# Kernel tuning notes

Measured on AMD Instinct MI355X. Metric: run time of the kernel, lower is better.

## Reference

```python
import jax, jax.numpy as jnp
import numpy as np

H = 512          # hidden_size
HALF = 256       # hidden_size // 2 (RGCN feature dim)
NHEAD = 8
NLAYER = 12
NBLOCK = 2
NENT = 50000
NREL = 12
NBASES = 8
NEDGE = 500000
TXTD = 768       # raw text/image feature dim
BATCH, ELEN, SLEN = 32, 50, 128


def setup_inputs() -> dict:
    key = jax.random.key(0)
    ks = jax.random.split(key, 40)
    def p(i, shape, scale=0.02):
        return jax.random.normal(ks[i], shape, jnp.float32) * scale
    inp = {
        'entity_ids': jax.random.randint(ks[0], (BATCH, ELEN), 0, NENT),
        'token_embeds': jax.random.normal(ks[1], (BATCH, SLEN, H), jnp.float32),
        'edge_index': jax.random.randint(ks[2], (2, NEDGE), 0, NENT),
        'edge_type': jax.random.randint(ks[3], (NEDGE,), 0, NREL),
        'node_embeds': p(4, (NENT, HALF)),
        'rgcn_basis': p(5, (NBASES, HALF, HALF)),
        'rgcn_comp': p(6, (NREL, NBASES), 0.3),
        'rgcn_root': p(7, (HALF, HALF)),
        'rgcn_bias': p(8, (HALF,)),
        'kg_proj_w': p(9, (HALF, H)), 'kg_proj_b': p(10, (H,)),
        'text_proj_w': p(11, (TXTD, H)), 'text_proj_b': p(12, (H,)),
        'image_proj_w': p(13, (TXTD, H)), 'image_proj_b': p(14, (H,)),
        'cq_w': p(15, (H, H)), 'cq_b': p(16, (H,)),
        'kgk_w': p(17, (H, H)), 'kgk_b': p(18, (H,)),
        'imk_w': p(19, (H, H)), 'imk_b': p(20, (H,)),
        'txk_w': p(21, (H, H)), 'txk_b': p(22, (H,)),
        'pp1_w1': p(23, (H, HALF)), 'pp1_b1': p(24, (HALF,)),
        'pp1_w2': p(25, (HALF, H)), 'pp1_b2': p(26, (H,)),
        'pp2_w': p(27, (H, NLAYER * NBLOCK * H)), 'pp2_b': p(28, (NLAYER * NBLOCK * H,)),
        'text_embeds_init': p(29, (NENT, TXTD), 1.0),
        'image_embeds_init': p(30, (NENT, TXTD), 1.0),
    }
    return inp


def _rgcn(x, edge_index, edge_type, basis, comp, root, bias):
    # PyG RGCNConv with basis decomposition, aggr='mean', root weight + bias.
    # mean_{e: rel=r, dst=i}(x[src_e] @ W_r) == (mean_{e}(x[src_e])) @ W_r, so we
    # aggregate raw features per (dst, relation) segment then apply W_r once per node.
    N = x.shape[0]
    src, dst = edge_index[0], edge_index[1]
    seg = dst * NREL + edge_type                      # combined (node, relation) key
    msgs = x[src]                                     # [E, HALF] gather
    agg = jax.ops.segment_sum(msgs, seg, num_segments=N * NREL)
    cnt = jax.ops.segment_sum(jnp.ones((src.shape[0],), x.dtype), seg, num_segments=N * NREL)
    mean = (agg / jnp.maximum(cnt, 1.0)[:, None]).reshape(N, NREL, HALF)
    w_rel = jnp.einsum('rb,bio->rio', comp, basis)    # [R, HALF, HALF]
    out = jnp.einsum('nri,rio->no', mean, w_rel) + x @ root + bias
    return out


def reference(entity_ids, token_embeds, edge_index, edge_type, node_embeds,
              rgcn_basis, rgcn_comp, rgcn_root, rgcn_bias,
              kg_proj_w, kg_proj_b, text_proj_w, text_proj_b,
              image_proj_w, image_proj_b, cq_w, cq_b,
              kgk_w, kgk_b, imk_w, imk_b, txk_w, txk_b,
              pp1_w1, pp1_b1, pp1_w2, pp1_b2, pp2_w, pp2_b,
              text_embeds_init, image_embeds_init):
    kg_all = _rgcn(node_embeds, edge_index, edge_type, rgcn_basis, rgcn_comp, rgcn_root, rgcn_bias)
    kg_all = kg_all @ kg_proj_w + kg_proj_b           # [N, H]
    kg_feat = kg_all[entity_ids]                      # [B, L, H]
    text_feat = text_embeds_init[entity_ids] @ text_proj_w + text_proj_b
    image_feat = image_embeds_init[entity_ids] @ image_proj_w + image_proj_b
    # context-guided fusion
    q = (jnp.mean(token_embeds, axis=1) @ cq_w + cq_b)[:, None, :]   # [B, 1, H]
    kg_s = jnp.sum(q * (kg_feat @ kgk_w + kgk_b), -1, keepdims=True)
    img_s = jnp.sum(q * (image_feat @ imk_w + imk_b), -1, keepdims=True)
    txt_s = jnp.sum(q * (text_feat @ txk_w + txk_b), -1, keepdims=True)
    w = jax.nn.softmax(jnp.concatenate([kg_s, img_s, txt_s], axis=-1), axis=-1)
    fused = w[..., 0:1] * kg_feat + w[..., 1:2] * image_feat + w[..., 2:3] * text_feat
    # prompt expansion
    h = jax.nn.relu(fused @ pp1_w1 + pp1_b1) @ pp1_w2 + pp1_b2 + fused
    p = h @ pp2_w + pp2_b                             # [B, L, NLAYER*NBLOCK*H]
    B, L = entity_ids.shape
    p = p.reshape(B, L, NLAYER, NBLOCK, NHEAD, H // NHEAD)
    p = jnp.transpose(p, (2, 3, 0, 4, 1, 5))          # [layer, block, B, head, L, head_dim]
    loss_cl = jnp.float32(0.0)                        # output_entity=False path
    return p, loss_cl
```

## Files before the change

### kernel.cpp

```cpp
#include <hip/hip_runtime.h>

#define HDIM 512
#define HALF 256
#define NRELS 12
#define NBASES 8
#define NLAYERS 12
#define NBLOCKS 2
#define NHEADS 8
#define NENTS 50000
#define TXTD 768
#define BATCH 32
#define ELEN 50
#define SLEN 128
#define NPOS (BATCH * ELEN)
#define NSEG (NPOS * NRELS)
#define BCAP 64

typedef unsigned short u16;
typedef __attribute__((ext_vector_type(8))) __bf16 bf16x8;
typedef __attribute__((ext_vector_type(4))) float f32x4;

__device__ __forceinline__ u16 f2bf(float f) {
    unsigned int u = __float_as_uint(f);
    unsigned int r = (u + 0x7FFFu + ((u >> 16) & 1u)) >> 16;
    return (u16)r;
}
__device__ __forceinline__ float bf2f(u16 v) {
    return __uint_as_float(((unsigned int)v) << 16);
}

#define ASYNC_COPY16(g, l)                                                              \
    __builtin_amdgcn_global_load_lds((const __attribute__((address_space(1))) void*)(g), \
                                     (__attribute__((address_space(3))) unsigned int*)(l), 16, 0, 0)

__global__ void init_kernel(int* __restrict__ map, int* __restrict__ segcnt,
                            int* __restrict__ nuniq, float* __restrict__ zb,
                            const float* __restrict__ kgb, const float* __restrict__ imb,
                            const float* __restrict__ txb, u16* __restrict__ SW,
                            const float* __restrict__ rgcn_bias,
                            const float* __restrict__ kg_proj_w,
                            const float* __restrict__ kg_proj_b,
                            float* __restrict__ biasC, float* __restrict__ out_last) {
    int blk = blockIdx.x;
    int t = threadIdx.x;
    if (blk >= 128) {
        int n = (blk - 128) * 256 + t;
        float acc = kg_proj_b[n];
        for (int c = 0; c < HALF; ++c) acc += rgcn_bias[c] * kg_proj_w[(size_t)c * HDIM + n];
        biasC[n] = acc;
        return;
    }
    int tid = blk * 256 + t;
    const int nt = 128 * 256;
    int4 m4 = {-1, -1, -1, -1};
    for (int i = tid; i < NENTS / 4; i += nt) ((int4*)map)[i] = m4;
    int4 z4 = {0, 0, 0, 0};
    for (int i = tid; i < NSEG / 4; i += nt) ((int4*)segcnt)[i] = z4;
    for (int i = tid; i < 2304; i += nt) zb[i] = 0.f;
    if (tid < HDIM) {
        SW[(size_t)1536 * HDIM + tid] = f2bf(kgb[tid]);
        SW[(size_t)1537 * HDIM + tid] = f2bf(imb[tid]);
        SW[(size_t)1538 * HDIM + tid] = f2bf(txb[tid]);
    }
    if (tid == 0) { *nuniq = 0; *out_last = 0.f; }
}

__global__ void dedup_kernel(const int* __restrict__ eid, int* __restrict__ map,
                             int* __restrict__ uniq, int* __restrict__ nuniq) {
    int i = blockIdx.x * blockDim.x + threadIdx.x;
    if (i >= NPOS) return;
    int n = eid[i];
    int old = atomicCAS(&map[n], -1, -2);
    if (old == -1) {
        int idx = atomicAdd(nuniq, 1);
        uniq[idx] = n;
        __threadfence();
        map[n] = idx;
    }
}

struct PrepArgs {
    const float* src[12];
    u16* dst[12];
};

__global__ __launch_bounds__(256) void midprep_kernel(
    const float* __restrict__ tok, u16* __restrict__ TMEAN,
    const int* __restrict__ uniq, const int* __restrict__ nuniq,
    const float* __restrict__ txi, const float* __restrict__ imi,
    u16* __restrict__ TXIN, u16* __restrict__ IMIN,
    const int* __restrict__ ei, const int* __restrict__ et, const int* __restrict__ map,
    int* __restrict__ segcnt, int* __restrict__ bucket, int E, PrepArgs a) {
    int blk = blockIdx.x;
    int t = threadIdx.x;
    if (blk < 64) {
        int b = blk >> 1;
        int col = (blk & 1) * 256 + t;
        float s = 0.f;
        for (int si = 0; si < SLEN; ++si) s += tok[((size_t)b * SLEN + si) * HDIM + col];
        TMEAN[(size_t)b * HDIM + col] = f2bf(s * (1.0f / SLEN));
    } else if (blk < 352) {
        if (t >= TXTD / 4) return;
        int nu = *nuniq;
        for (int u = blk - 64; u < NPOS; u += 288) {
            if (u >= nu) {
                ushort4 z = {0, 0, 0, 0};
                ((ushort4*)(TXIN + (size_t)u * TXTD))[t] = z;
                ((ushort4*)(IMIN + (size_t)u * TXTD))[t] = z;
                continue;
            }
            int n = uniq[u];
            float4 v = ((const float4*)(txi + (size_t)n * TXTD))[t];
            ushort4 o;
            o.x = f2bf(v.x); o.y = f2bf(v.y); o.z = f2bf(v.z); o.w = f2bf(v.w);
            ((ushort4*)(TXIN + (size_t)u * TXTD))[t] = o;
            v = ((const float4*)(imi + (size_t)n * TXTD))[t];
            o.x = f2bf(v.x); o.y = f2bf(v.y); o.z = f2bf(v.z); o.w = f2bf(v.w);
            ((ushort4*)(IMIN + (size_t)u * TXTD))[t] = o;
        }
    } else if (blk < 1024) {
        const int* __restrict__ dstA = ei + E;
        int tid0 = (blk - 352) * 256 + t;
        const int stride = 672 * 256;
        for (int e = tid0; e < E; e += stride) {
            int c = map[dstA[e]];
            if (c >= 0) {
                int seg = c * NRELS + et[e];
                int p = atomicAdd(&segcnt[seg], 1);
                if (p < BCAP) bucket[seg * BCAP + p] = ei[e];
            }
        }
    } else {
        constexpr int NN[7]  = {512, 512, 512, 256, 512, 12288, 512};
        constexpr int LDT[7] = {256, 768, 768, 512, 256, 512, 512};
        constexpr int BASE[13] = {0, 128, 512, 896, 1024, 1152, 7296,
                                  7552, 8064, 8128, 8384, 8640, 8896};
        __shared__ u16 tb[32][33];
        int bid = blk - 1024;
        int op = 0;
        #pragma unroll
        for (int i = 1; i < 12; ++i)
            if (bid >= BASE[i]) op = i;
        int idx = bid - BASE[op];
        if (op < 7) {
            int Nv = 0, ldt = 0;
            #pragma unroll
            for (int i = 0; i < 7; ++i)
                if (op == i) { Nv = NN[i]; ldt = LDT[i]; }
            int ncols = Nv / 32;
            int n0 = (idx % ncols) * 32, k0 = (idx / ncols) * 32;
            const float* W = a.src[op];
            u16* WT = a.dst[op];
            int tx = t & 31, ty = t >> 5;
            #pragma unroll
            for (int i = ty; i < 32; i += 8)
                tb[i][tx] = f2bf(W[(size_t)(k0 + i) * Nv + n0 + tx]);
            __syncthreads();
            #pragma unroll
            for (int i = ty; i < 32; i += 8)
                WT[(size_t)(n0 + i) * ldt + k0 + tx] = tb[tx][i];
        } else {
            int e = idx * 1024 + t * 4;
            float4 v = *(const float4*)(a.src[op] + e);
            ushort4 o;
            o.x = f2bf(v.x); o.y = f2bf(v.y); o.z = f2bf(v.z); o.w = f2bf(v.w);
            *(ushort4*)(a.dst[op] + e) = o;
        }
    }
}

template <int BM, int BN, int WM, int WN, bool SCATTER>
__device__ __forceinline__ void gemm_body(const u16* __restrict__ A, const u16* __restrict__ BT,
                                          const float* __restrict__ bias,
                                          void* __restrict__ Cout, int M, int N, int K,
                                          int bx, int by, bool outbf) {
    constexpr int MF = WM / 16, NF = WN / 16;
    constexpr int NWC = BN / WN;
    __shared__ u16 ldsA[BM][64];
    __shared__ u16 ldsB[BN][64];
    const int tid = threadIdx.x;
    const int lane = tid & 63;
    const int wv = tid >> 6;
    const int m0 = by * BM;
    const int n0 = bx * BN;
    const int wr = wv / NWC, wc = wv % NWC;
    const int srow = lane >> 3;
    const int sslot = lane & 7;

    f32x4 acc[MF][NF];
    #pragma unroll
    for (int i = 0; i < MF; ++i)
        #pragma unroll
        for (int j = 0; j < NF; ++j)
            #pragma unroll
            for (int r = 0; r < 4; ++r) acc[i][j][r] = 0.f;

    for (int k0 = 0; k0 < K; k0 += 64) {
        #pragma unroll
        for (int i = 0; i < BM / 32; ++i) {
            int R = wv * (BM / 4) + i * 8 + srow;
            int gm = m0 + R;
            gm = gm < M ? gm : M - 1;
            int s = sslot ^ (R & 7);
            ASYNC_COPY16(A + (size_t)gm * K + k0 + s * 8, &ldsA[wv * (BM / 4) + i * 8][0]);
        }
        #pragma unroll
        for (int i = 0; i < BN / 32; ++i) {
            int R = wv * (BN / 4) + i * 8 + srow;
            int s = sslot ^ (R & 7);
            ASYNC_COPY16(BT + (size_t)(n0 + R) * K + k0 + s * 8, &ldsB[wv * (BN / 4) + i * 8][0]);
        }
        __syncthreads();
        #pragma unroll
        for (int ks = 0; ks < 2; ++ks) {
            bf16x8 af[MF], bf[NF];
            int kg = ks * 4 + (lane >> 4);
            int rl = lane & 15;
            #pragma unroll
            for (int i = 0; i < MF; ++i) {
                int row = wr * WM + i * 16 + rl;
                af[i] = *(const bf16x8*)&ldsA[row][(kg ^ (row & 7)) * 8];
            }
            #pragma unroll
            for (int j = 0; j < NF; ++j) {
                int row = wc * WN + j * 16 + rl;
                bf[j] = *(const bf16x8*)&ldsB[row][(kg ^ (row & 7)) * 8];
            }
            #pragma unroll
            for (int i = 0; i < MF; ++i)
                #pragma unroll
                for (int j = 0; j < NF; ++j)
                    acc[i][j] = __builtin_amdgcn_mfma_f32_16x16x32_bf16(af[i], bf[j], acc[i][j], 0, 0, 0);
        }
        __syncthreads();
    }

    const int rl = lane & 15, rg = lane >> 4;
    #pragma unroll
    for (int i = 0; i < MF; ++i) {
        #pragma unroll
        for (int j = 0; j < NF; ++j) {
            int col = n0 + wc * WN + j * 16 + rl;
            float bv = bias[col];
            #pragma unroll
            for (int r = 0; r < 4; ++r) {
                int row = m0 + wr * WM + i * 16 + rg * 4 + r;
                if (row >= M) continue;
                float x = acc[i][j][r] + bv;
                if (SCATTER) {
                    int layer = col >> 10, blk = (col >> 9) & 1, head = (col >> 6) & 7, hd = col & 63;
                    int bb = row / ELEN, ll = row - bb * ELEN;
                    size_t oi = (((((size_t)layer * NBLOCKS + blk) * BATCH + bb) * NHEADS + head) * ELEN + ll) * 64 + hd;
                    ((float*)Cout)[oi] = x;
                } else if (outbf) {
                    ((u16*)Cout)[(size_t)row * N + col] = f2bf(x);
                } else {
                    ((float*)Cout)[(size_t)row * N + col] = x;
                }
            }
        }
    }
}

__global__ __launch_bounds__(256) void build_kernel(
    const int* __restrict__ segcnt, const int* __restrict__ bucket,
    const int* __restrict__ uniq, const int* __restrict__ nuniq,
    const float* __restrict__ comp, const float* __restrict__ x, u16* __restrict__ MBX,
    const u16* __restrict__ TMEAN, const u16* __restrict__ CQT,
    const float* __restrict__ cq_b, u16* __restrict__ QB,
    const u16* __restrict__ KGT, const u16* __restrict__ W1f,
    const float* __restrict__ ZB, u16* __restrict__ WC) {
    int blk = blockIdx.x;
    if (blk >= NPOS) {
        const u16 *A, *BT;
        const float* bias;
        u16* C;
        int M, N, K, bx, by;
        if (blk >= NPOS + 8) {
            int i = blk - (NPOS + 8);
            A = KGT; BT = W1f; bias = ZB; C = WC;
            M = HDIM; N = 2304; K = HALF; bx = i % 36; by = i / 36;
        } else {
            A = TMEAN; BT = CQT; bias = cq_b; C = QB;
            M = BATCH; N = HDIM; K = HDIM; bx = blk - NPOS; by = 0;
        }
        gemm_body<64, 64, 32, 32, false>(A, BT, bias, C, M, N, K, bx, by, true);
        return;
    }
    int u = blk;
    int i = threadIdx.x;
    __shared__ float sc[NRELS * NBASES];
    if (i < NRELS * NBASES) sc[i] = comp[i];
    __syncthreads();
    u16* row = MBX + (size_t)u * 2304;
    int nu = *nuniq;
    if (u >= nu) {
        for (int b = 0; b < NBASES + 1; ++b) row[b * HALF + i] = 0;
        return;
    }
    float mr[NRELS];
    #pragma unroll
    for (int r = 0; r < NRELS; ++r) {
        int seg = u * NRELS + r;
        int c = segcnt[seg];
        int n = min(c, BCAP);
        float acc = 0.f;
        for (int e = 0; e < n; ++e) {
            int s = bucket[seg * BCAP + e];
            acc += x[(size_t)s * HALF + i];
        }
        mr[r] = acc * (1.f / fmaxf((float)c, 1.f));
    }
    #pragma unroll
    for (int b = 0; b < NBASES; ++b) {
        float a = 0.f;
        #pragma unroll
        for (int r = 0; r < NRELS; ++r) a += sc[r * NBASES + b] * mr[r];
        row[b * HALF + i] = f2bf(a);
    }
    row[NBASES * HALF + i] = f2bf(x[(size_t)uniq[u] * HALF + i]);
}

struct Proj4Args {
    const u16 *MBX, *WC, *TXIN, *TXT, *IMIN, *IMT, *QB, *SW;
    const float *biasC, *txb, *imb, *ZB;
    u16 *KGU, *TXU, *IMU;
    float* QP;
};
__global__ __launch_bounds__(256) void proj4_kernel(Proj4Args a) {
    int b = blockIdx.x;
    const u16 *A, *BT;
    const float* bias;
    void* C;
    int M, N, K, bx, by;
    bool obf;
    if (b < 200) {
        A = a.MBX; BT = a.WC; bias = a.biasC; C = a.KGU;
        M = NPOS; N = HDIM; K = 2304; bx = b % 8; by = b / 8; obf = true;
    } else if (b < 400) {
        int i = b - 200;
        A = a.TXIN; BT = a.TXT; bias = a.txb; C = a.TXU;
        M = NPOS; N = HDIM; K = TXTD; bx = i % 8; by = i / 8; obf = true;
    } else if (b < 600) {
        int i = b - 400;
        A = a.IMIN; BT = a.IMT; bias = a.imb; C = a.IMU;
        M = NPOS; N = HDIM; K = TXTD; bx = i % 8; by = i / 8; obf = true;
    } else {
        A = a.QB; BT = a.SW; bias = a.ZB; C = a.QP;
        M = BATCH; N = 1600; K = HDIM; bx = b - 600; by = 0; obf = false;
    }
    gemm_body<64, 64, 32, 32, false>(A, BT, bias, C, M, N, K, bx, by, obf);
}

__global__ __launch_bounds__(256) void tail_kernel(
    const int* __restrict__ eid, const int* __restrict__ map,
    const u16* __restrict__ KGU, const u16* __restrict__ IMU, const u16* __restrict__ TXU,
    const float* __restrict__ qp,
    const u16* __restrict__ W1T, const float* __restrict__ pp1_b1,
    const u16* __restrict__ W2T, const float* __restrict__ pp1_b2,
    u16* __restrict__ Hh) {
    __shared__ u16 FUS[16][520];
    __shared__ u16 P1s[16][264];
    const int bm0 = blockIdx.x * 16;
    const int lane = threadIdx.x & 63;
    const int wv = threadIdx.x >> 6;

    for (int rr = wv; rr < 16; rr += 4) {
        int bl = bm0 + rr;
        int b = bl / ELEN;
        int u = map[eid[bl]];
        const u16* kg = KGU + (size_t)u * HDIM;
        const u16* im = IMU + (size_t)u * HDIM;
        const u16* tx = TXU + (size_t)u * HDIM;
        const float* qrow = qp + (size_t)b * 1600;
        float pkg = 0.f, pim = 0.f, ptx = 0.f;
        for (int e = lane; e < HDIM; e += 64) {
            pkg += bf2f(kg[e]) * qrow[e];
            pim += bf2f(im[e]) * qrow[512 + e];
            ptx += bf2f(tx[e]) * qrow[1024 + e];
        }
        #pragma unroll
        for (int off = 32; off; off >>= 1) {
            pkg += __shfl_down(pkg, off);
            pim += __shfl_down(pim, off);
            ptx += __shfl_down(ptx, off);
        }
        float w0, w1, w2;
        if (lane == 0) {
            float av = pkg + qrow[1536];
            float c1 = pim + qrow[1537];
            float c2 = ptx + qrow[1538];
            float mx = fmaxf(av, fmaxf(c1, c2));
            float ea = __expf(av - mx), eb = __expf(c1 - mx), ec = __expf(c2 - mx);
            float inv = 1.f / (ea + eb + ec);
            w0 = ea * inv; w1 = eb * inv; w2 = ec * inv;
        }
        w0 = __shfl(w0, 0); w1 = __shfl(w1, 0); w2 = __shfl(w2, 0);
        for (int e = lane; e < HDIM; e += 64) {
            float v = w0 * bf2f(kg[e]) + w1 * bf2f(im[e]) + w2 * bf2f(tx[e]);
            FUS[rr][e] = f2bf(v);
        }
    }
    __syncthreads();

    {
        const int rl = lane & 15;
        const int kgrp = lane >> 4;
        f32x4 acc[4];
        #pragma unroll
        for (int j = 0; j < 4; ++j)
            #pragma unroll
            for (int r = 0; r < 4; ++r) acc[j][r] = 0.f;
        for (int kk = 0; kk < 512; kk += 32) {
            int k8 = kk + kgrp * 8;
            bf16x8 af = *(const bf16x8*)&FUS[rl][k8];
            bf16x8 bf[4];
            #pragma unroll
            for (int j = 0; j < 4; ++j) {
                int n = wv * 64 + j * 16 + rl;
                bf[j] = *(const bf16x8*)&W1T[(size_t)n * 512 + k8];
            }
            #pragma unroll
            for (int j = 0; j < 4; ++j)
                acc[j] = __builtin_amdgcn_mfma_f32_16x16x32_bf16(af, bf[j], acc[j], 0, 0, 0);
        }
        const int rg = lane >> 4;
        #pragma unroll
        for (int j = 0; j < 4; ++j) {
            int col = wv * 64 + j * 16 + rl;
            float bv = pp1_b1[col];
            #pragma unroll
            for (int r = 0; r < 4; ++r) {
                int row = rg * 4 + r;
                P1s[row][col] = f2bf(fmaxf(acc[j][r] + bv, 0.f));
            }
        }
    }
    __syncthreads();

    {
        const int rl = lane & 15;
        const int kgrp = lane >> 4;
        f32x4 acc[8];
        #pragma unroll
        for (int j = 0; j < 8; ++j)
            #pragma unroll
            for (int r = 0; r < 4; ++r) acc[j][r] = 0.f;
        for (int kk = 0; kk < 256; kk += 32) {
            int k8 = kk + kgrp * 8;
            bf16x8 af = *(const bf16x8*)&P1s[rl][k8];
            bf16x8 bf[8];
            #pragma unroll
            for (int j = 0; j < 8; ++j) {
                int n = wv * 128 + j * 16 + rl;
                bf[j] = *(const bf16x8*)&W2T[(size_t)n * 256 + k8];
            }
            #pragma unroll
            for (int j = 0; j < 8; ++j)
                acc[j] = __builtin_amdgcn_mfma_f32_16x16x32_bf16(af, bf[j], acc[j], 0, 0, 0);
        }
        const int rg = lane >> 4;
        #pragma unroll
        for (int j = 0; j < 8; ++j) {
            int col = wv * 128 + j * 16 + rl;
            float bv = pp1_b2[col];
            #pragma unroll
            for (int r = 0; r < 4; ++r) {
                int row = rg * 4 + r;
                float v = acc[j][r] + bv + bf2f(FUS[row][col]);
                Hh[(size_t)(bm0 + row) * HDIM + col] = f2bf(v);
            }
        }
    }
}

__global__ __launch_bounds__(256)
void pp2_kernel(const u16* __restrict__ A, const u16* __restrict__ BT,
                const float* __restrict__ bias, void* __restrict__ Cout,
                int M, int N, int K) {
    gemm_body<128, 128, 64, 64, true>(A, BT, bias, Cout, M, N, K, blockIdx.x, blockIdx.y, false);
}

extern "C" void kernel_launch(void* const* d_in, const int* in_sizes, int n_in,
                              void* d_out, int out_size, void* d_ws, size_t ws_size,
                              hipStream_t stream) {
    const int* entity_ids = (const int*)d_in[0];
    const float* token_embeds = (const float*)d_in[1];
    const int* edge_index = (const int*)d_in[2];
    const int* edge_type = (const int*)d_in[3];
    const float* node_embeds = (const float*)d_in[4];
    const float* rgcn_basis = (const float*)d_in[5];
    const float* rgcn_comp = (const float*)d_in[6];
    const float* rgcn_root = (const float*)d_in[7];
    const float* rgcn_bias = (const float*)d_in[8];
    const float* kg_proj_w = (const float*)d_in[9];
    const float* kg_proj_b = (const float*)d_in[10];
    const float* text_proj_w = (const float*)d_in[11];
    const float* text_proj_b = (const float*)d_in[12];
    const float* image_proj_w = (const float*)d_in[13];
    const float* image_proj_b = (const float*)d_in[14];
    const float* cq_w = (const float*)d_in[15];
    const float* cq_b = (const float*)d_in[16];
    const float* kgk_w = (const float*)d_in[17];
    const float* imk_w = (const float*)d_in[19];
    const float* txk_w = (const float*)d_in[21];
    const float* pp1_w1 = (const float*)d_in[23];
    const float* pp1_b1 = (const float*)d_in[24];
    const float* pp1_w2 = (const float*)d_in[25];
    const float* pp1_b2 = (const float*)d_in[26];
    const float* pp2_w = (const float*)d_in[27];
    const float* pp2_b = (const float*)d_in[28];
    const float* text_init = (const float*)d_in[29];
    const float* image_init = (const float*)d_in[30];

    const int E = in_sizes[3];

    size_t off = 0;
    auto alloc = [&](size_t bytes) { size_t o = off; off += (bytes + 255) & ~(size_t)255; return o; };
    char* ws = (char*)d_ws;
    size_t map_o  = alloc((size_t)NENTS * 4);
    size_t nun_o  = alloc(4);
    size_t unq_o  = alloc((size_t)NPOS * 4);
    size_t scnt_o = alloc((size_t)NSEG * 4);
    size_t bkt_o  = alloc((size_t)NSEG * BCAP * 4);
    size_t mbx_o  = alloc((size_t)NPOS * 2304 * 2);
    size_t w1f_o  = alloc((size_t)2304 * HALF * 2);
    size_t wc_o   = alloc((size_t)HDIM * 2304 * 2);
    size_t bc_o   = alloc((size_t)HDIM * 4);
    size_t kgt_o  = alloc((size_t)HDIM * HALF * 2);
    size_t kgu_o  = alloc((size_t)NPOS * HDIM * 2);
    size_t txin_o = alloc((size_t)NPOS * TXTD * 2);
    size_t imin_o = alloc((size_t)NPOS * TXTD * 2);
    size_t txt_o  = alloc((size_t)HDIM * TXTD * 2);
    size_t imt_o  = alloc((size_t)HDIM * TXTD * 2);
    size_t txu_o  = alloc((size_t)NPOS * HDIM * 2);
    size_t imu_o  = alloc((size_t)NPOS * HDIM * 2);
    size_t tm_o   = alloc((size_t)BATCH * HDIM * 2);
    size_t qb_o   = alloc((size_t)BATCH * HDIM * 2);
    size_t cqt_o  = alloc((size_t)HDIM * HDIM * 2);
    size_t sw_o   = alloc((size_t)1600 * HDIM * 2);
    size_t qp_o   = alloc((size_t)BATCH * 1600 * 4);
    size_t zb_o   = alloc((size_t)2304 * 4);
    size_t w1t_o  = alloc((size_t)HALF * HDIM * 2);
    size_t w2t_o  = alloc((size_t)HDIM * HALF * 2);
    size_t h_o    = alloc((size_t)NPOS * HDIM * 2);
    size_t pp2t_o = alloc((size_t)12288 * HDIM * 2);
    if (off > ws_size) return;

    int* map = (int*)(ws + map_o);
    int* nuniq = (int*)(ws + nun_o);
    int* uniq = (int*)(ws + unq_o);
    int* segcnt = (int*)(ws + scnt_o);
    int* bucket = (int*)(ws + bkt_o);
    u16* MBX = (u16*)(ws + mbx_o);
    u16* W1f = (u16*)(ws + w1f_o);
    u16* WC  = (u16*)(ws + wc_o);
    float* biasC = (float*)(ws + bc_o);
    u16* KGT = (u16*)(ws + kgt_o);
    u16* KGU = (u16*)(ws + kgu_o);
    u16* TXIN = (u16*)(ws + txin_o);
    u16* IMIN = (u16*)(ws + imin_o);
    u16* TXT = (u16*)(ws + txt_o);
    u16* IMT = (u16*)(ws + imt_o);
    u16* TXU = (u16*)(ws + txu_o);
    u16* IMU = (u16*)(ws + imu_o);
    u16* TMEAN = (u16*)(ws + tm_o);
    u16* QB  = (u16*)(ws + qb_o);
    u16* CQT = (u16*)(ws + cqt_o);
    u16* SW  = (u16*)(ws + sw_o);
    float* QP  = (float*)(ws + qp_o);
    float* ZB  = (float*)(ws + zb_o);
    u16* W1T = (u16*)(ws + w1t_o);
    u16* W2T = (u16*)(ws + w2t_o);
    u16* Hh  = (u16*)(ws + h_o);
    u16* PP2T = (u16*)(ws + pp2t_o);
    float* OUT = (float*)d_out;

    init_kernel<<<130, 256, 0, stream>>>(map, segcnt, nuniq, ZB,
                                         (const float*)d_in[18], (const float*)d_in[20],
                                         (const float*)d_in[22], SW,
                                         rgcn_bias, kg_proj_w, kg_proj_b, biasC,
                                         OUT + (out_size - 1));
    dedup_kernel<<<(NPOS + 255) / 256, 256, 0, stream>>>(entity_ids, map, uniq, nuniq);
    PrepArgs pa;
    pa.src[0] = kg_proj_w;    pa.dst[0] = KGT;
    pa.src[1] = text_proj_w;  pa.dst[1] = TXT;
    pa.src[2] = image_proj_w; pa.dst[2] = IMT;
    pa.src[3] = pp1_w1;       pa.dst[3] = W1T;
    pa.src[4] = pp1_w2;       pa.dst[4] = W2T;
    pa.src[5] = pp2_w;        pa.dst[5] = PP2T;
    pa.src[6] = cq_w;         pa.dst[6] = CQT;
    pa.src[7] = rgcn_basis;   pa.dst[7] = W1f;
    pa.src[8] = rgcn_root;    pa.dst[8] = W1f + (size_t)2048 * HALF;
    pa.src[9] = kgk_w;        pa.dst[9] = SW;
    pa.src[10] = imk_w;       pa.dst[10] = SW + (size_t)HDIM * HDIM;
    pa.src[11] = txk_w;       pa.dst[11] = SW + (size_t)2 * HDIM * HDIM;
    midprep_kernel<<<9920, 256, 0, stream>>>(token_embeds, TMEAN,
                                             uniq, nuniq, text_init, image_init, TXIN, IMIN,
                                             edge_index, edge_type, map, segcnt, bucket, E, pa);
    build_kernel<<<NPOS + 8 + 288, 256, 0, stream>>>(segcnt, bucket, uniq, nuniq, rgcn_comp,
                                                     node_embeds, MBX, TMEAN, CQT, cq_b, QB,
                                                     KGT, W1f, ZB, WC);
    Proj4Args p4;
    p4.MBX = MBX; p4.WC = WC; p4.biasC = biasC; p4.KGU = KGU;
    p4.TXIN = TXIN; p4.TXT = TXT; p4.txb = text_proj_b; p4.TXU = TXU;
    p4.IMIN = IMIN; p4.IMT = IMT; p4.imb = image_proj_b; p4.IMU = IMU;
    p4.QB = QB; p4.SW = SW; p4.ZB = ZB; p4.QP = QP;
    proj4_kernel<<<625, 256, 0, stream>>>(p4);
    tail_kernel<<<NPOS / 16, 256, 0, stream>>>(entity_ids, map, KGU, IMU, TXU, QP,
                                               W1T, pp1_b1, W2T, pp1_b2, Hh);
    pp2_kernel<<<dim3(12288 / 128, (NPOS + 127) / 128), 256, 0, stream>>>(
        Hh, PP2T, pp2_b, OUT, NPOS, 12288, HDIM);
}
```

Before: 153.9 us.

## Move text/image projections into build kernel and XCD-swizzle pp2 grid

The text and image projection GEMMs move from the proj kernel into the build kernel, where they run alongside the RGCN aggregation blocks. The proj kernel now only does the KG projection and the score projection, so it is shorter and no longer has to wait on these independent GEMMs. The pp2 GEMM now uses a 1D grid remapped so that each XCD gets a contiguous range of N-columns, which should improve L2 reuse of the B operand. The risk is that the larger build launch adds tail imbalance, and the swizzle assumes blocks are dispatched round-robin across 8 XCDs.

```diff
diff --git a/kernel.cpp b/kernel.cpp
--- a/kernel.cpp
+++ b/kernel.cpp
@@ -262,26 +262,41 @@
     }
 }
 
-__global__ __launch_bounds__(256) void build_kernel(
-    const int* __restrict__ segcnt, const int* __restrict__ bucket,
-    const int* __restrict__ uniq, const int* __restrict__ nuniq,
-    const float* __restrict__ comp, const float* __restrict__ x, u16* __restrict__ MBX,
-    const u16* __restrict__ TMEAN, const u16* __restrict__ CQT,
-    const float* __restrict__ cq_b, u16* __restrict__ QB,
-    const u16* __restrict__ KGT, const u16* __restrict__ W1f,
-    const float* __restrict__ ZB, u16* __restrict__ WC) {
+struct BuildArgs {
+    const int *segcnt, *bucket, *uniq, *nuniq;
+    const float *comp, *x;
+    u16* MBX;
+    const u16 *TMEAN, *CQT;
+    const float* cq_b;
+    u16* QB;
+    const u16 *KGT, *W1f;
+    const float* ZB;
+    u16* WC;
+    const u16 *TXIN, *TXT, *IMIN, *IMT;
+    const float *txb, *imb;
+    u16 *TXU, *IMU;
+};
+__global__ __launch_bounds__(256) void build_kernel(BuildArgs a) {
     int blk = blockIdx.x;
     if (blk >= NPOS) {
         const u16 *A, *BT;
         const float* bias;
         u16* C;
         int M, N, K, bx, by;
-        if (blk >= NPOS + 8) {
+        if (blk >= NPOS + 8 + 288 + 200) {
+            int i = blk - (NPOS + 8 + 288 + 200);
+            A = a.IMIN; BT = a.IMT; bias = a.imb; C = a.IMU;
+            M = NPOS; N = HDIM; K = TXTD; bx = i % 8; by = i / 8;
+        } else if (blk >= NPOS + 8 + 288) {
+            int i = blk - (NPOS + 8 + 288);
+            A = a.TXIN; BT = a.TXT; bias = a.txb; C = a.TXU;
+            M = NPOS; N = HDIM; K = TXTD; bx = i % 8; by = i / 8;
+        } else if (blk >= NPOS + 8) {
             int i = blk - (NPOS + 8);
-            A = KGT; BT = W1f; bias = ZB; C = WC;
+            A = a.KGT; BT = a.W1f; bias = a.ZB; C = a.WC;
             M = HDIM; N = 2304; K = HALF; bx = i % 36; by = i / 36;
         } else {
-            A = TMEAN; BT = CQT; bias = cq_b; C = QB;
+            A = a.TMEAN; BT = a.CQT; bias = a.cq_b; C = a.QB;
             M = BATCH; N = HDIM; K = HDIM; bx = blk - NPOS; by = 0;
         }
         gemm_body<64, 64, 32, 32, false>(A, BT, bias, C, M, N, K, bx, by, true);
@@ -290,10 +305,10 @@
     int u = blk;
     int i = threadIdx.x;
     __shared__ float sc[NRELS * NBASES];
-    if (i < NRELS * NBASES) sc[i] = comp[i];
+    if (i < NRELS * NBASES) sc[i] = a.comp[i];
     __syncthreads();
-    u16* row = MBX + (size_t)u * 2304;
-    int nu = *nuniq;
+    u16* row = a.MBX + (size_t)u * 2304;
+    int nu = *a.nuniq;
     if (u >= nu) {
         for (int b = 0; b < NBASES + 1; ++b) row[b * HALF + i] = 0;
         return;
@@ -302,54 +317,40 @@
     #pragma unroll
     for (int r = 0; r < NRELS; ++r) {
         int seg = u * NRELS + r;
-        int c = segcnt[seg];
+        int c = a.segcnt[seg];
         int n = min(c, BCAP);
         float acc = 0.f;
         for (int e = 0; e < n; ++e) {
-            int s = bucket[seg * BCAP + e];
-            acc += x[(size_t)s * HALF + i];
+            int s = a.bucket[seg * BCAP + e];
+            acc += a.x[(size_t)s * HALF + i];
         }
         mr[r] = acc * (1.f / fmaxf((float)c, 1.f));
     }
     #pragma unroll
     for (int b = 0; b < NBASES; ++b) {
-        float a = 0.f;
-        #pragma unroll
-        for (int r = 0; r < NRELS; ++r) a += sc[r * NBASES + b] * mr[r];
-        row[b * HALF + i] = f2bf(a);
-    }
-    row[NBASES * HALF + i] = f2bf(x[(size_t)uniq[u] * HALF + i]);
-}
-
-struct Proj4Args {
-    const u16 *MBX, *WC, *TXIN, *TXT, *IMIN, *IMT, *QB, *SW;
-    const float *biasC, *txb, *imb, *ZB;
-    u16 *KGU, *TXU, *IMU;
+        float v = 0.f;
+        #pragma unroll
+        for (int r = 0; r < NRELS; ++r) v += sc[r * NBASES + b] * mr[r];
+        row[b * HALF + i] = f2bf(v);
+    }
+    row[NBASES * HALF + i] = f2bf(a.x[(size_t)a.uniq[u] * HALF + i]);
+}
+
+struct ProjArgs {
+    const u16 *MBX, *WC, *QB, *SW;
+    const float *biasC, *ZB;
+    u16* KGU;
     float* QP;
 };
-__global__ __launch_bounds__(256) void proj4_kernel(Proj4Args a) {
+__global__ __launch_bounds__(256) void proj_kernel(ProjArgs a) {
     int b = blockIdx.x;
-    const u16 *A, *BT;
-    const float* bias;
-    void* C;
-    int M, N, K, bx, by;
-    bool obf;
     if (b < 200) {
-        A = a.MBX; BT = a.WC; bias = a.biasC; C = a.KGU;
-        M = NPOS; N = HDIM; K = 2304; bx = b % 8; by = b / 8; obf = true;
-    } else if (b < 400) {
-        int i = b - 200;
-        A = a.TXIN; BT = a.TXT; bias = a.txb; C = a.TXU;
-        M = NPOS; N = HDIM; K = TXTD; bx = i % 8; by = i / 8; obf = true;
-    } else if (b < 600) {
-        int i = b - 400;
-        A = a.IMIN; BT = a.IMT; bias = a.imb; C = a.IMU;
-        M = NPOS; N = HDIM; K = TXTD; bx = i % 8; by = i / 8; obf = true;
+        gemm_body<64, 64, 32, 32, false>(a.MBX, a.WC, a.biasC, a.KGU,
+                                         NPOS, HDIM, 2304, b % 8, b / 8, true);
     } else {
-        A = a.QB; BT = a.SW; bias = a.ZB; C = a.QP;
-        M = BATCH; N = 1600; K = HDIM; bx = b - 600; by = 0; obf = false;
-    }
-    gemm_body<64, 64, 32, 32, false>(A, BT, bias, C, M, N, K, bx, by, obf);
+        gemm_body<64, 64, 32, 32, false>(a.QB, a.SW, a.ZB, a.QP,
+                                         BATCH, 1600, HDIM, b - 200, 0, false);
+    }
 }
 
 __global__ __launch_bounds__(256) void tail_kernel(
@@ -478,7 +479,12 @@
 void pp2_kernel(const u16* __restrict__ A, const u16* __restrict__ BT,
                 const float* __restrict__ bias, void* __restrict__ Cout,
                 int M, int N, int K) {
-    gemm_body<128, 128, 64, 64, true>(A, BT, bias, Cout, M, N, K, blockIdx.x, blockIdx.y, false);
+    int id = blockIdx.x;
+    int xcd = id & 7;
+    int local = id >> 3;
+    int bx = xcd * 12 + local % 12;
+    int by = local / 12;
+    gemm_body<128, 128, 64, 64, true>(A, BT, bias, Cout, M, N, K, bx, by, false);
 }
 
 extern "C" void kernel_launch(void* const* d_in, const int* in_sizes, int n_in,
@@ -598,17 +604,19 @@
     midprep_kernel<<<9920, 256, 0, stream>>>(token_embeds, TMEAN,
                                              uniq, nuniq, text_init, image_init, TXIN, IMIN,
                                              edge_index, edge_type, map, segcnt, bucket, E, pa);
-    build_kernel<<<NPOS + 8 + 288, 256, 0, stream>>>(segcnt, bucket, uniq, nuniq, rgcn_comp,
-                                                     node_embeds, MBX, TMEAN, CQT, cq_b, QB,
-                                                     KGT, W1f, ZB, WC);
-    Proj4Args p4;
-    p4.MBX = MBX; p4.WC = WC; p4.biasC = biasC; p4.KGU = KGU;
-    p4.TXIN = TXIN; p4.TXT = TXT; p4.txb = text_proj_b; p4.TXU = TXU;
-    p4.IMIN = IMIN; p4.IMT = IMT; p4.imb = image_proj_b; p4.IMU = IMU;
-    p4.QB = QB; p4.SW = SW; p4.ZB = ZB; p4.QP = QP;
-    proj4_kernel<<<625, 256, 0, stream>>>(p4);
+    BuildArgs ba;
+    ba.segcnt = segcnt; ba.bucket = bucket; ba.uniq = uniq; ba.nuniq = nuniq;
+    ba.comp = rgcn_comp; ba.x = node_embeds; ba.MBX = MBX;
+    ba.TMEAN = TMEAN; ba.CQT = CQT; ba.cq_b = cq_b; ba.QB = QB;
+    ba.KGT = KGT; ba.W1f = W1f; ba.ZB = ZB; ba.WC = WC;
+    ba.TXIN = TXIN; ba.TXT = TXT; ba.IMIN = IMIN; ba.IMT = IMT;
+    ba.txb = text_proj_b; ba.imb = image_proj_b; ba.TXU = TXU; ba.IMU = IMU;
+    build_kernel<<<NPOS + 8 + 288 + 400, 256, 0, stream>>>(ba);
+    ProjArgs pr;
+    pr.MBX = MBX; pr.WC = WC; pr.biasC = biasC; pr.KGU = KGU;
+    pr.QB = QB; pr.SW = SW; pr.ZB = ZB; pr.QP = QP;
+    proj_kernel<<<225, 256, 0, stream>>>(pr);
     tail_kernel<<<NPOS / 16, 256, 0, stream>>>(entity_ids, map, KGU, IMU, TXU, QP,
                                                W1T, pp1_b1, W2T, pp1_b2, Hh);
-    pp2_kernel<<<dim3(12288 / 128, (NPOS + 127) / 128), 256, 0, stream>>>(
-        Hh, PP2T, pp2_b, OUT, NPOS, 12288, HDIM);
-}
+    pp2_kernel<<<1248, 256, 0, stream>>>(Hh, PP2T, pp2_b, OUT, NPOS, 12288, HDIM);
+}
```

Measured after the change: 155.3 us. About the same (+0.9%).
